# Optimization experiments

Measured on AMD Instinct MI355X. Metric: run time of the kernel, lower is better.

## Reference

```python
import jax, jax.numpy as jnp
import numpy as np

N_NODES = 100000
N_EDGES = 1600000
IN_FEATS = 256
OUT_DIM = 128


def setup_inputs() -> dict:
    key = jax.random.key(0)
    k_x, k_e, k_w = jax.random.split(key, 3)
    x = jax.random.normal(k_x, (N_NODES, IN_FEATS), dtype=jnp.float32)
    edge_index = jax.random.randint(k_e, (2, N_EDGES), 0, N_NODES, dtype=jnp.int64)
    # Glorot-ish init for the GCN weight
    W = jax.random.normal(k_w, (IN_FEATS, OUT_DIM), dtype=jnp.float32) * (1.0 / np.sqrt(IN_FEATS))
    b = jnp.zeros((OUT_DIM,), dtype=jnp.float32)
    return {"x": x, "edge_index": edge_index, "W": W, "b": b}


def reference(x, edge_index, W, b):
    N = x.shape[0]
    # GCN with self-loops and symmetric normalization (PyG gcn_norm)
    self_loops = jnp.arange(N, dtype=edge_index.dtype)
    row = jnp.concatenate([edge_index[0], self_loops])  # source nodes
    col = jnp.concatenate([edge_index[1], self_loops])  # target nodes
    deg = jnp.zeros((N,), dtype=x.dtype).at[col].add(1.0)
    deg_inv_sqrt = jnp.where(deg > 0, jax.lax.rsqrt(jnp.maximum(deg, 1.0)), 0.0)
    norm = deg_inv_sqrt[row] * deg_inv_sqrt[col]  # [E+N]
    # Linear transform first (small GEMM), then sparse aggregation
    h = x @ W + b                                  # [N, out_dim]
    msg = h[row] * norm[:, None]                   # gather + scale, [E+N, out_dim]
    out = jax.ops.segment_sum(msg, col, num_segments=N)  # scatter-add
    # relu; dropout is identity in eval mode
    return jax.nn.relu(out)
```

## Files before the change

kernel.cpp:

```cpp
#include <hip/hip_runtime.h>

typedef __attribute__((ext_vector_type(8))) short short8;
typedef __attribute__((ext_vector_type(4))) float f32x4;
typedef unsigned int u32;

#define IN_F 256
#define OUT_F 128
#define NPB 128
#define NBUK 782
#define MAXCAP 2560

__device__ __forceinline__ float bf2f(u32 u16) {
    union { u32 i; float f; } v; v.i = u16 << 16; return v.f;
}
__device__ __forceinline__ float asf(u32 u) {
    union { u32 i; float f; } v; v.i = u; return v.f;
}
__device__ __forceinline__ unsigned short f2bf(float f) {
    union { float f; u32 i; } v; v.f = f;
    u32 u = v.i;
    return (unsigned short)((u + 0x7fffu + ((u >> 16) & 1u)) >> 16);
}

__global__ __launch_bounds__(256) void k_transposeW(const float* __restrict__ W,
                                                    unsigned short* __restrict__ Wt,
                                                    unsigned short* __restrict__ hb,
                                                    int* __restrict__ bcur, int N) {
    int idx = blockIdx.x * 256 + threadIdx.x;
    if (idx < IN_F * OUT_F) {
        int k = idx >> 7;
        int n = idx & 127;
        int ct = n >> 4, mm = n & 15;
        int i = k >> 5, q = (k >> 3) & 3, e = k & 7;
        int d = (ct * 8 + i) * 64 + q * 16 + mm;
        Wt[(size_t)d * 8 + e] = f2bf(W[idx]);
    }
    if (idx < OUT_F) hb[(size_t)N * OUT_F + idx] = 0;
    if (idx < NBUK) bcur[idx] = 0;
}

__global__ __launch_bounds__(512) void k_bin(const int* __restrict__ row, const int* __restrict__ col,
                                             int* __restrict__ bcur, int* __restrict__ ebuf,
                                             int E, int chunk) {
    __shared__ int hist[NBUK];
    __shared__ int cbase[NBUK];
    __shared__ u32 epk[3200];
    __shared__ unsigned short ebk[3200];
    int t = threadIdx.x;
    int e0 = blockIdx.x * chunk;
    int e1 = e0 + chunk; if (e1 > E) e1 = E;
    int cnt = e1 - e0;

    for (int i = t; i < NBUK; i += 512) hist[i] = 0;
    __syncthreads();
    for (int i = e0 + t; i < e1; i += 512) {
        int c = col[i];
        int r = row[i];
        int j = i - e0;
        int b = c >> 7;
        epk[j] = ((u32)r << 7) | (u32)(c & 127);
        ebk[j] = (unsigned short)b;
        atomicAdd(&hist[b], 1);
    }
    __syncthreads();
    for (int i = t; i < NBUK; i += 512) {
        int h = hist[i];
        cbase[i] = h ? atomicAdd(&bcur[i], h) : 0;
        hist[i] = 0;
    }
    __syncthreads();
    for (int j = t; j < cnt; j += 512) {
        u32 p = epk[j];
        int b = ebk[j];
        int pos = atomicAdd(&hist[b], 1) + cbase[b];
        ebuf[(size_t)b * MAXCAP + pos] = (int)p;
    }
}

__global__ __launch_bounds__(512) void k_fine(const int* __restrict__ bcur, const int* __restrict__ ebuf,
                                              int* __restrict__ offs, int* __restrict__ deg,
                                              float* __restrict__ dis, int* __restrict__ srci, int N) {
    __shared__ int dl[NPB];
    __shared__ int sc[NPB];
    int b = blockIdx.x;
    int t = threadIdx.x;
    int count = bcur[b];
    const int* eb = ebuf + (size_t)b * MAXCAP;

    if (t < NPB) dl[t] = 0;
    __syncthreads();
    for (int i = t; i < count; i += 512)
        atomicAdd(&dl[eb[i] & 127], 1);
    __syncthreads();
    int myDeg = (t < NPB) ? dl[t] : 0;
    if (t < NPB) sc[t] = myDeg;
    __syncthreads();
    for (int off = 1; off < NPB; off <<= 1) {
        int a = (t >= off && t < NPB) ? sc[t - off] : 0;
        __syncthreads();
        if (t < NPB) sc[t] += a;
        __syncthreads();
    }
    int bbase = b * MAXCAP;
    if (t < NPB) {
        int excl = sc[t] - myDeg;
        int node = b * NPB + t;
        if (node < N) {
            offs[node] = bbase + excl;
            deg[node] = myDeg;
            dis[node] = rsqrtf((float)myDeg + 1.0f);
        }
        dl[t] = excl;
    }
    __syncthreads();
    for (int i = t; i < count; i += 512) {
        int p = eb[i];
        int pos = atomicAdd(&dl[p & 127], 1);
        srci[bbase + pos] = p >> 7;
    }
}

__global__ __launch_bounds__(256) void k_gemm(const float* __restrict__ x,
                                              const unsigned short* __restrict__ Wt,
                                              const float* __restrict__ bias,
                                              const float* __restrict__ dis,
                                              unsigned short* __restrict__ hb, int nrows) {
    __shared__ short8 WB[4096];
    int wave = threadIdx.x >> 6;
    int lane = threadIdx.x & 63;
    int m = lane & 15;
    int quad = lane >> 4;

    int row0 = blockIdx.x * 64 + wave * 16;
    int nm1 = nrows - 1;
    int r = row0 + m; if (r > nm1) r = nm1;
    const float4* px = (const float4*)(x + (size_t)r * IN_F);

    float4 xa[16];
#pragma unroll
    for (int i = 0; i < 8; i++) {
        xa[2 * i]     = px[8 * i + 2 * quad];
        xa[2 * i + 1] = px[8 * i + 2 * quad + 1];
    }

    {
        const char* gb = (const char*)Wt;
        char* lb = (char*)WB;
#pragma unroll
        for (int s = 0; s < 16; s++) {
            int d = (wave * 16 + s) * 64;
            __builtin_amdgcn_global_load_lds(
                (const __attribute__((address_space(1))) u32*)(gb + (size_t)(d + lane) * 16),
                (__attribute__((address_space(3))) u32*)(lb + (size_t)d * 16),
                16, 0, 0);
        }
    }

    float bv[8];
#pragma unroll
    for (int ct = 0; ct < 8; ct++) bv[ct] = bias[ct * 16 + m];

    __syncthreads();

    f32x4 acc[8];
#pragma unroll
    for (int ct = 0; ct < 8; ct++) acc[ct] = (f32x4){0.f, 0.f, 0.f, 0.f};

#pragma unroll
    for (int i = 0; i < 8; i++) {
        float4 a0 = xa[2 * i], a1 = xa[2 * i + 1];
        short8 af;
        af[0] = (short)f2bf(a0.x); af[1] = (short)f2bf(a0.y);
        af[2] = (short)f2bf(a0.z); af[3] = (short)f2bf(a0.w);
        af[4] = (short)f2bf(a1.x); af[5] = (short)f2bf(a1.y);
        af[6] = (short)f2bf(a1.z); af[7] = (short)f2bf(a1.w);
#pragma unroll
        for (int ct = 0; ct < 8; ct++) {
            short8 w = WB[ct * 512 + i * 64 + lane];
            acc[ct] = __builtin_amdgcn_mfma_f32_16x16x32_bf16(af, w, acc[ct], 0, 0, 0);
        }
    }

    int orow0 = row0 + quad * 4;
#pragma unroll
    for (int rr = 0; rr < 4; rr++) {
        int orow = orow0 + rr;
        if (orow < nrows) {
            float dr = dis[orow];
#pragma unroll
            for (int ct = 0; ct < 8; ct++)
                hb[(size_t)orow * OUT_F + ct * 16 + m] = f2bf((acc[ct][rr] + bv[ct]) * dr);
        }
    }
}

__global__ __launch_bounds__(256) void k_agg(const unsigned short* __restrict__ hb,
                                             const float* __restrict__ dis,
                                             const int* __restrict__ offs, const int* __restrict__ deg,
                                             const int* __restrict__ srci,
                                             float* __restrict__ out, int n) {
    int wid = threadIdx.x >> 6;
    int node = __builtin_amdgcn_readfirstlane(blockIdx.x * 4 + wid);
    if (node >= n) return;
    int lane = threadIdx.x & 63;

    int start = offs[node];
    int cnt   = deg[node];
    const int* sl = srci + start;

    u32 v = *(const u32*)(hb + (size_t)node * OUT_F + lane * 2);
    float ax = bf2f(v & 0xffffu);
    float ay = bf2f(v >> 16);

    for (int j = 0; j < cnt; j += 8) {
        int rr[8];
#pragma unroll
        for (int k = 0; k < 8; k++)
            rr[k] = (j + k < cnt) ? sl[j + k] : n;
        u32 w[8];
#pragma unroll
        for (int k = 0; k < 8; k++)
            w[k] = *(const u32*)(hb + (size_t)rr[k] * OUT_F + lane * 2);
#pragma unroll
        for (int k = 0; k < 8; k++) {
            ax += asf(w[k] << 16);
            ay += asf(w[k] & 0xffff0000u);
        }
    }

    float di = dis[node];
    float2 o;
    o.x = fmaxf(ax * di, 0.f);
    o.y = fmaxf(ay * di, 0.f);
    *(float2*)(out + (size_t)node * OUT_F + lane * 2) = o;
}

static inline size_t alignup(size_t v, size_t a) { return (v + a - 1) & ~(a - 1); }

extern "C" void kernel_launch(void* const* d_in, const int* in_sizes, int n_in,
                              void* d_out, int out_size, void* d_ws, size_t ws_size,
                              hipStream_t stream) {
    const float* x  = (const float*)d_in[0];
    const int* ei   = (const int*)d_in[1];
    const float* W  = (const float*)d_in[2];
    const float* b  = (const float*)d_in[3];
    float* out      = (float*)d_out;

    const int N = in_sizes[0] / IN_F;
    const int E = in_sizes[1] / 2;
    const int* rowp = ei;
    const int* colp = ei + E;

    char* ws = (char*)d_ws;
    size_t off = 0;
    int*   bcur   = (int*)(ws + off);   off = alignup(off + (size_t)NBUK * 4, 256);
    int*   deg    = (int*)(ws + off);   off = alignup(off + (size_t)N * 4, 256);
    float* dis    = (float*)(ws + off); off = alignup(off + (size_t)N * 4, 256);
    int*   offs   = (int*)(ws + off);   off = alignup(off + (size_t)N * 4, 256);
    unsigned short* Wt = (unsigned short*)(ws + off); off = alignup(off + (size_t)IN_F * OUT_F * 2, 256);
    int*   ebuf   = (int*)(ws + off);   off = alignup(off + (size_t)NBUK * MAXCAP * 4, 256);
    int*   srci   = (int*)(ws + off);   off = alignup(off + ((size_t)NBUK * MAXCAP + 64) * 4, 256);
    unsigned short* hb = (unsigned short*)(ws + off); off = alignup(off + (size_t)(N + 1) * OUT_F * 2, 256);

    k_transposeW<<<(IN_F * OUT_F + 255) / 256, 256, 0, stream>>>(W, Wt, hb, bcur, N);

    int chunk = (E + 511) / 512;
    k_bin<<<512, 512, 0, stream>>>(rowp, colp, bcur, ebuf, E, chunk);
    k_fine<<<NBUK, 512, 0, stream>>>(bcur, ebuf, offs, deg, dis, srci, N);

    k_gemm<<<(N + 63) / 64, 256, 0, stream>>>(x, Wt, b, dis, hb, N);

    k_agg<<<(N + 3) / 4, 256, 0, stream>>>(hb, dis, offs, deg, srci, out, N);
}
```

Before: 272.7 us.

## Split aggregation into two feature-half passes and fold W transpose into binning

The aggregation kernel now runs twice, each pass gathering one 64-feature half of the bf16 hidden matrix with one element per lane. The aim is to shrink each pass's working set so it caches better. In exchange, neighbor index lists are read twice and each gather is narrower. The weight transpose/convert is folded into extra blocks of the binning kernel, and a memset replaces the bucket-counter zeroing, which saves a launch.

```diff
diff --git a/kernel.cpp b/kernel.cpp
--- a/kernel.cpp
+++ b/kernel.cpp
@@ -13,40 +13,37 @@
 __device__ __forceinline__ float bf2f(u32 u16) {
     union { u32 i; float f; } v; v.i = u16 << 16; return v.f;
 }
-__device__ __forceinline__ float asf(u32 u) {
-    union { u32 i; float f; } v; v.i = u; return v.f;
-}
 __device__ __forceinline__ unsigned short f2bf(float f) {
     union { float f; u32 i; } v; v.f = f;
     u32 u = v.i;
     return (unsigned short)((u + 0x7fffu + ((u >> 16) & 1u)) >> 16);
 }
 
-__global__ __launch_bounds__(256) void k_transposeW(const float* __restrict__ W,
-                                                    unsigned short* __restrict__ Wt,
-                                                    unsigned short* __restrict__ hb,
-                                                    int* __restrict__ bcur, int N) {
-    int idx = blockIdx.x * 256 + threadIdx.x;
-    if (idx < IN_F * OUT_F) {
-        int k = idx >> 7;
-        int n = idx & 127;
-        int ct = n >> 4, mm = n & 15;
-        int i = k >> 5, q = (k >> 3) & 3, e = k & 7;
-        int d = (ct * 8 + i) * 64 + q * 16 + mm;
-        Wt[(size_t)d * 8 + e] = f2bf(W[idx]);
-    }
-    if (idx < OUT_F) hb[(size_t)N * OUT_F + idx] = 0;
-    if (idx < NBUK) bcur[idx] = 0;
-}
-
 __global__ __launch_bounds__(512) void k_bin(const int* __restrict__ row, const int* __restrict__ col,
                                              int* __restrict__ bcur, int* __restrict__ ebuf,
+                                             const float* __restrict__ W, unsigned short* __restrict__ Wt,
+                                             unsigned short* __restrict__ hb, int N,
                                              int E, int chunk) {
     __shared__ int hist[NBUK];
     __shared__ int cbase[NBUK];
     __shared__ u32 epk[3200];
     __shared__ unsigned short ebk[3200];
     int t = threadIdx.x;
+
+    if (blockIdx.x >= 512) {
+        int idx = (blockIdx.x - 512) * 512 + t;
+        if (idx < IN_F * OUT_F) {
+            int k = idx >> 7;
+            int n = idx & 127;
+            int ct = n >> 4, mm = n & 15;
+            int i = k >> 5, q = (k >> 3) & 3, e = k & 7;
+            int d = (ct * 8 + i) * 64 + q * 16 + mm;
+            Wt[(size_t)d * 8 + e] = f2bf(W[idx]);
+        }
+        if (idx < OUT_F) hb[(size_t)N * OUT_F + idx] = 0;
+        return;
+    }
+
     int e0 = blockIdx.x * chunk;
     int e1 = e0 + chunk; if (e1 > E) e1 = E;
     int cnt = e1 - e0;
@@ -198,19 +195,19 @@
                                              const float* __restrict__ dis,
                                              const int* __restrict__ offs, const int* __restrict__ deg,
                                              const int* __restrict__ srci,
-                                             float* __restrict__ out, int n) {
+                                             float* __restrict__ out, int n, int pass) {
     int wid = threadIdx.x >> 6;
     int node = __builtin_amdgcn_readfirstlane(blockIdx.x * 4 + wid);
     if (node >= n) return;
     int lane = threadIdx.x & 63;
+    int fb = pass * 64 + lane;
+    const unsigned short* hp = hb + fb;
 
     int start = offs[node];
     int cnt   = deg[node];
     const int* sl = srci + start;
 
-    u32 v = *(const u32*)(hb + (size_t)node * OUT_F + lane * 2);
-    float ax = bf2f(v & 0xffffu);
-    float ay = bf2f(v >> 16);
+    float ax = bf2f(hp[(size_t)node * OUT_F]);
 
     for (int j = 0; j < cnt; j += 8) {
         int rr[8];
@@ -220,19 +217,14 @@
         u32 w[8];
 #pragma unroll
         for (int k = 0; k < 8; k++)
-            w[k] = *(const u32*)(hb + (size_t)rr[k] * OUT_F + lane * 2);
-#pragma unroll
-        for (int k = 0; k < 8; k++) {
-            ax += asf(w[k] << 16);
-            ay += asf(w[k] & 0xffff0000u);
-        }
+            w[k] = hp[(size_t)rr[k] * OUT_F];
+#pragma unroll
+        for (int k = 0; k < 8; k++)
+            ax += bf2f(w[k]);
     }
 
     float di = dis[node];
-    float2 o;
-    o.x = fmaxf(ax * di, 0.f);
-    o.y = fmaxf(ay * di, 0.f);
-    *(float2*)(out + (size_t)node * OUT_F + lane * 2) = o;
+    out[(size_t)node * OUT_F + fb] = fmaxf(ax * di, 0.f);
 }
 
 static inline size_t alignup(size_t v, size_t a) { return (v + a - 1) & ~(a - 1); }
@@ -262,13 +254,14 @@
     int*   srci   = (int*)(ws + off);   off = alignup(off + ((size_t)NBUK * MAXCAP + 64) * 4, 256);
     unsigned short* hb = (unsigned short*)(ws + off); off = alignup(off + (size_t)(N + 1) * OUT_F * 2, 256);
 
-    k_transposeW<<<(IN_F * OUT_F + 255) / 256, 256, 0, stream>>>(W, Wt, hb, bcur, N);
+    (void)hipMemsetAsync(bcur, 0, (size_t)NBUK * 4, stream);
 
     int chunk = (E + 511) / 512;
-    k_bin<<<512, 512, 0, stream>>>(rowp, colp, bcur, ebuf, E, chunk);
+    k_bin<<<576, 512, 0, stream>>>(rowp, colp, bcur, ebuf, W, Wt, hb, N, E, chunk);
     k_fine<<<NBUK, 512, 0, stream>>>(bcur, ebuf, offs, deg, dis, srci, N);
 
     k_gemm<<<(N + 63) / 64, 256, 0, stream>>>(x, Wt, b, dis, hb, N);
 
-    k_agg<<<(N + 3) / 4, 256, 0, stream>>>(hb, dis, offs, deg, srci, out, N);
-}
+    k_agg<<<(N + 3) / 4, 256, 0, stream>>>(hb, dis, offs, deg, srci, out, N, 0);
+    k_agg<<<(N + 3) / 4, 256, 0, stream>>>(hb, dis, offs, deg, srci, out, N, 1);
+}
```

After: 299.9 us. 1.1x slower.
